# Performance work log

Measured on AMD Instinct MI355X. Metric: run time of the kernel, lower is better.

Reference implementation:

```python
import jax, jax.numpy as jnp
import numpy as np

N, E, G = 50000, 800000, 64
IN, EDGE = 128, 16
HID, H = 32, 4
FHID, HF = 64, 4
OUT = 16
NEG_SLOPE = 0.2


def _segment_softmax(logits, seg, num):
    m = jax.ops.segment_max(logits, seg, num_segments=num)
    m = jnp.where(jnp.isfinite(m), m, 0.0)
    p = jnp.exp(logits - m[seg])
    s = jax.ops.segment_sum(p, seg, num_segments=num)
    return p / (s[seg] + 1e-16)


def gatv2(x, src, dst, eattr, Wl, bl, Wr, br, We, att, bias, concat):
    # PyG GATv2Conv with add_self_loops=True (edge_attr fill_value='mean')
    n = x.shape[0]
    heads, ch = att.shape
    ones = jnp.ones((src.shape[0],), x.dtype)
    cnt = jax.ops.segment_sum(ones, dst, num_segments=n)
    mean_attr = jax.ops.segment_sum(eattr, dst, num_segments=n) / jnp.maximum(cnt, 1.0)[:, None]
    loop = jnp.arange(n)
    s = jnp.concatenate([src, loop])
    d = jnp.concatenate([dst, loop])
    ea = jnp.concatenate([eattr, mean_attr], axis=0)
    xl = (x @ Wl + bl).reshape(n, heads, ch)   # lin_l (source)
    xr = (x @ Wr + br).reshape(n, heads, ch)   # lin_r (target)
    ee = (ea @ We).reshape(-1, heads, ch)      # lin_edge (no bias)
    z = jax.nn.leaky_relu(xl[s] + xr[d] + ee, NEG_SLOPE)  # [E+N, H, C]
    logits = jnp.einsum('ehc,hc->eh', z, att)
    alpha = _segment_softmax(logits, d, n)
    out = jax.ops.segment_sum(alpha[:, :, None] * xl[s], d, num_segments=n)  # [N, H, C]
    out = out.reshape(n, heads * ch) if concat else out.mean(axis=1)
    return out + bias


def _forward(x, edge_attr, src, dst, batch,
             Wl0, bl0, Wr0, br0, We0, att0, bo0,
             Wlh, blh, Wrh, brh, Weh, atth, boh,
             Wlf, blf, Wrf, brf, Wef, attf, bof,
             Wlin, blin):
    h1 = jax.nn.relu(gatv2(x, src, dst, edge_attr, Wl0, bl0, Wr0, br0, We0, att0, bo0, True))
    h2 = jax.nn.relu(gatv2(h1, src, dst, edge_attr, Wlh, blh, Wrh, brh, Weh, atth, boh, True))
    h3 = jax.nn.relu(gatv2(h2, src, dst, edge_attr, Wlf, blf, Wrf, brf, Wef, attf, bof, False))
    # global_mean_pool over graphs
    gsum = jax.ops.segment_sum(h3, batch, num_segments=G)
    gcnt = jax.ops.segment_sum(jnp.ones((h3.shape[0],), h3.dtype), batch, num_segments=G)
    g = gsum / jnp.maximum(gcnt, 1.0)[:, None]
    return g @ Wlin + blin  # final_dropout inactive in eval mode


def setup_inputs():
    key = jax.random.key(0)
    ks = jax.random.split(key, 20)
    def p(i, shape, fan_in):
        return jax.random.normal(ks[i], shape, jnp.float32) / np.sqrt(fan_in)
    z = lambda *s: jnp.zeros(s, jnp.float32)
    return {
        'x': jax.random.normal(ks[0], (N, IN), jnp.float32),
        'edge_index': jax.random.randint(ks[1], (2, E), 0, N),
        'batch': jnp.sort(jax.random.randint(ks[2], (N,), 0, G)),
        'edge_attr': jax.random.normal(ks[3], (E, EDGE), jnp.float32),
        'Wl0': p(4, (IN, H * HID), IN), 'bl0': z(H * HID),
        'Wr0': p(5, (IN, H * HID), IN), 'br0': z(H * HID),
        'We0': p(6, (EDGE, H * HID), EDGE), 'att0': p(7, (H, HID), HID), 'bo0': z(H * HID),
        'Wlh': p(8, (H * HID, H * HID), H * HID), 'blh': z(H * HID),
        'Wrh': p(9, (H * HID, H * HID), H * HID), 'brh': z(H * HID),
        'Weh': p(10, (EDGE, H * HID), EDGE), 'atth': p(11, (H, HID), HID), 'boh': z(H * HID),
        'Wlf': p(12, (H * HID, HF * FHID), H * HID), 'blf': z(HF * FHID),
        'Wrf': p(13, (H * HID, HF * FHID), H * HID), 'brf': z(HF * FHID),
        'Wef': p(14, (EDGE, HF * FHID), EDGE), 'attf': p(15, (HF, FHID), FHID), 'bof': z(FHID),
        'Wlin': p(16, (FHID, OUT), FHID), 'blin': z(OUT),
    }


def reference(x, edge_index, batch, edge_attr, Wl0, bl0, Wr0, br0, We0, att0, bo0, Wlh, blh, Wrh, brh, Weh, atth, boh, Wlf, blf, Wrf, brf, Wef, attf, bof, Wlin, blin):
    return _forward(x, edge_attr, edge_index[0], edge_index[1], batch,
                    Wl0, bl0, Wr0, br0, We0, att0, bo0,
                    Wlh, blh, Wrh, brh, Weh, atth, boh,
                    Wlf, blf, Wrf, brf, Wef, attf, bof,
                    Wlin, blin)
```

## Files before the change

kernel.cpp:

```cpp
#include <hip/hip_runtime.h>
#include <cstddef>

#define NSLOPE 0.2f

constexpr int NN = 50000;
constexpr int EE = 800000;
constexpr int GG = 64;
constexpr int SCAN_B = 1024;

typedef unsigned short ushort_t;
typedef unsigned int uint_t;
typedef __bf16 bhalf;
typedef bhalf bhalf8 __attribute__((ext_vector_type(8)));
typedef float floatx4 __attribute__((ext_vector_type(4)));
typedef _Float16 half_t;
typedef half_t half2_t __attribute__((ext_vector_type(2)));

__device__ __forceinline__ ushort_t f2b(float f) {
  unsigned int u = __float_as_uint(f);
  unsigned int r = (u + 0x7fffu + ((u >> 16) & 1u)) >> 16;
  return (ushort_t)r;
}
__device__ __forceinline__ float b2f(ushort_t b) {
  return __uint_as_float(((unsigned int)b) << 16);
}
__device__ __forceinline__ uint_t packh2(float a, float b) {
  half2_t h = {(half_t)a, (half_t)b};
  return __builtin_bit_cast(uint_t, h);
}
__device__ __forceinline__ float dot2acc(uint_t ea, half2_t w, float c) {
  half2_t a = __builtin_bit_cast(half2_t, ea);
#if __has_builtin(__builtin_amdgcn_fdot2)
  return __builtin_amdgcn_fdot2(a, w, c, false);
#else
  return c + (float)a.x * (float)w.x + (float)a.y * (float)w.y;
#endif
}

__global__ void hist_kernel(const int* __restrict__ dst, int* __restrict__ hist, int E) {
  int e = blockIdx.x * blockDim.x + threadIdx.x;
  if (e < E) atomicAdd(&hist[dst[e]], 1);
}

__global__ void scan_block_kernel(const int* __restrict__ in, int* __restrict__ out,
                                  int* __restrict__ bsum, int n) {
  __shared__ int tmp[SCAN_B];
  int gid = blockIdx.x * SCAN_B + threadIdx.x;
  int v = (gid < n) ? in[gid] : 0;
  tmp[threadIdx.x] = v;
  __syncthreads();
  for (int off = 1; off < SCAN_B; off <<= 1) {
    int t = (threadIdx.x >= off) ? tmp[threadIdx.x - off] : 0;
    __syncthreads();
    tmp[threadIdx.x] += t;
    __syncthreads();
  }
  if (gid < n) out[gid] = tmp[threadIdx.x];
  if (threadIdx.x == SCAN_B - 1) bsum[blockIdx.x] = tmp[threadIdx.x];
}

__global__ void scan_totals_kernel(const int* __restrict__ bsum, int* __restrict__ boff, int nb) {
  if (blockIdx.x == 0 && threadIdx.x == 0) {
    int run = 0;
    for (int i = 0; i < nb; ++i) { boff[i] = run; run += bsum[i]; }
  }
}

__global__ void add_offsets_kernel(int* __restrict__ rowptr, const int* __restrict__ boff,
                                   int* __restrict__ cursor, int n) {
  int gid = blockIdx.x * SCAN_B + threadIdx.x;
  if (gid == 0) { rowptr[0] = 0; cursor[0] = 0; }
  if (gid < n) {
    int v = rowptr[1 + gid] + boff[blockIdx.x];
    rowptr[1 + gid] = v;
    if (1 + gid < n) cursor[1 + gid] = v;
  }
}

__global__ void scatter_fused_kernel(const int* __restrict__ dst, const int* __restrict__ src,
                                     const float* __restrict__ eattr, int* __restrict__ cursor,
                                     int* __restrict__ srcp, uint_t* __restrict__ eah, int E) {
  int e = blockIdx.x * blockDim.x + threadIdx.x;
  if (e >= E) return;
  const float4* a = reinterpret_cast<const float4*>(eattr + (size_t)e * 16);
  float4 f0 = a[0], f1 = a[1], f2 = a[2], f3 = a[3];
  int pos = atomicAdd(&cursor[dst[e]], 1);
  srcp[pos] = src[e];
  uint4 o0 = make_uint4(packh2(f0.x, f0.y), packh2(f0.z, f0.w),
                        packh2(f1.x, f1.y), packh2(f1.z, f1.w));
  uint4 o1 = make_uint4(packh2(f2.x, f2.y), packh2(f2.z, f2.w),
                        packh2(f3.x, f3.y), packh2(f3.z, f3.w));
  uint4* b = reinterpret_cast<uint4*>(eah + (size_t)pos * 8);
  b[0] = o0; b[1] = o1;
}

__global__ __launch_bounds__(256) void mean_attr_kernel(
    const int* __restrict__ rowptr, const uint_t* __restrict__ eah,
    uint_t* __restrict__ meanattr_h, int N) {
  const int lane = threadIdx.x & 63;
  int d = blockIdx.x * (blockDim.x >> 6) + (threadIdx.x >> 6);
  if (d >= N) return;
  int beg = rowptr[d], end = rowptr[d + 1];
  int k2 = lane & 7;
  int sub = lane >> 3;
  float ax = 0.f, ay = 0.f;
  for (int j = beg + sub; j < end; j += 8) {
    half2_t h = __builtin_bit_cast(half2_t, eah[(size_t)j * 8 + k2]);
    ax += (float)h.x; ay += (float)h.y;
  }
  ax += __shfl_xor(ax, 8);  ay += __shfl_xor(ay, 8);
  ax += __shfl_xor(ax, 16); ay += __shfl_xor(ay, 16);
  ax += __shfl_xor(ax, 32); ay += __shfl_xor(ay, 32);
  if (sub == 0) {
    int c = end - beg; if (c < 1) c = 1;
    float inv = 1.f / (float)c;
    meanattr_h[(size_t)d * 8 + k2] = packh2(ax * inv, ay * inv);
  }
}

__global__ void f2b_kernel(const float* __restrict__ in, ushort_t* __restrict__ out, int n4) {
  int i = blockIdx.x * blockDim.x + threadIdx.x;
  if (i >= n4) return;
  float4 v = reinterpret_cast<const float4*>(in)[i];
  ushort4 o = make_ushort4(f2b(v.x), f2b(v.y), f2b(v.z), f2b(v.w));
  reinterpret_cast<ushort4*>(out)[i] = o;
}

__global__ void prep_w_kernel(const float* W0, ushort_t* T0, int n0,
                              const float* W1, ushort_t* T1, int n1,
                              const float* W2, ushort_t* T2, int n2,
                              const float* W3, ushort_t* T3, int n3,
                              const float* W4, ushort_t* T4, int n4,
                              const float* W5, ushort_t* T5, int n5) {
  const float* W; ushort_t* T; int Nc;
  switch (blockIdx.y) {
    case 0: W = W0; T = T0; Nc = n0; break;
    case 1: W = W1; T = T1; Nc = n1; break;
    case 2: W = W2; T = T2; Nc = n2; break;
    case 3: W = W3; T = T3; Nc = n3; break;
    case 4: W = W4; T = T4; Nc = n4; break;
    default: W = W5; T = T5; Nc = n5; break;
  }
  int idx = blockIdx.x * blockDim.x + threadIdx.x;
  if (idx >= Nc * 128) return;
  int n = idx >> 7, k = idx & 127;
  T[idx] = f2b(W[(size_t)k * Nc + n]);
}

__global__ void prep_we_kernel(const float* We0, const float* att0, uint_t* w0, float* a0,
                               const float* We1, const float* att1, uint_t* w1, float* a1,
                               const float* We2, const float* att2, uint_t* w2, float* a2) {
  const float* We; const float* att; uint_t* wp; float* ap; int C;
  switch (blockIdx.y) {
    case 0: We = We0; att = att0; wp = w0; ap = a0; C = 128; break;
    case 1: We = We1; att = att1; wp = w1; ap = a1; C = 128; break;
    default: We = We2; att = att2; wp = w2; ap = a2; C = 256; break;
  }
  int idx = blockIdx.x * blockDim.x + threadIdx.x;
  if (idx >= 9 * C) return;
  if (idx < 8 * C) {
    int sh = (C == 256) ? 8 : 7;
    int k2 = idx >> sh, ch = idx & (C - 1);
    wp[idx] = packh2(We[(size_t)(2 * k2) * C + ch], We[(size_t)(2 * k2 + 1) * C + ch]);
  } else {
    int ch = idx - 8 * C;
    ap[ch] = att[ch] * 1.44269504f;
  }
}

__global__ __launch_bounds__(256) void gemm_bt_dual_bf16(
    const ushort_t* __restrict__ Xb,
    const ushort_t* __restrict__ Wt0, const float* __restrict__ b0, ushort_t* __restrict__ Y0,
    const ushort_t* __restrict__ Wt1, const float* __restrict__ b1, ushort_t* __restrict__ Y1,
    int M, int Nc) {
  constexpr int K = 128, BM = 128, LDT = 136;
  __shared__ ushort_t Als[BM * LDT];
  __shared__ ushort_t Bls[BM * LDT];
  int nb = Nc >> 7;
  int half = blockIdx.y / nb;
  int cb = blockIdx.y % nb;
  const ushort_t* Wt = half ? Wt1 : Wt0;
  const float* bias = half ? b1 : b0;
  ushort_t* Y = half ? Y1 : Y0;
  int r0 = blockIdx.x * BM;
  int col0 = cb * 128;
  int tid = threadIdx.x;
  {
    int rl = tid >> 5;
    int kq = (tid & 31) * 4;
#pragma unroll
    for (int s = 0; s < 16; ++s) {
      int row = rl + s * 8;
      int grow = r0 + row;
      ushort4 v = make_ushort4(0, 0, 0, 0);
      if (grow < M) v = *reinterpret_cast<const ushort4*>(Xb + (size_t)grow * K + kq);
      *reinterpret_cast<ushort4*>(&Als[row * LDT + kq]) = v;
      ushort4 wv = *reinterpret_cast<const ushort4*>(Wt + (size_t)(col0 + row) * K + kq);
      *reinterpret_cast<ushort4*>(&Bls[row * LDT + kq]) = wv;
    }
  }
  __syncthreads();
  int lane = tid & 63;
  int w = tid >> 6;
  int m0 = (w >> 1) * 64;
  int n0 = (w & 1) * 64;
  int rin = lane & 15, quad = lane >> 4;
  floatx4 acc[4][4];
#pragma unroll
  for (int i = 0; i < 4; ++i)
#pragma unroll
    for (int j = 0; j < 4; ++j) acc[i][j] = (floatx4){0.f, 0.f, 0.f, 0.f};
#pragma unroll
  for (int kt = 0; kt < 4; ++kt) {
    int ko = kt * 32 + quad * 8;
    bhalf8 af[4], bf[4];
#pragma unroll
    for (int i = 0; i < 4; ++i)
      af[i] = *reinterpret_cast<const bhalf8*>(&Als[(m0 + i * 16 + rin) * LDT + ko]);
#pragma unroll
    for (int i = 0; i < 4; ++i)
      bf[i] = *reinterpret_cast<const bhalf8*>(&Bls[(n0 + i * 16 + rin) * LDT + ko]);
#pragma unroll
    for (int mi = 0; mi < 4; ++mi)
#pragma unroll
      for (int ni = 0; ni < 4; ++ni)
        acc[mi][ni] = __builtin_amdgcn_mfma_f32_16x16x32_bf16(af[mi], bf[ni], acc[mi][ni], 0, 0, 0);
  }
#pragma unroll
  for (int ni = 0; ni < 4; ++ni) {
    int gcol = col0 + n0 + ni * 16 + rin;
    float bb = bias[gcol];
#pragma unroll
    for (int mi = 0; mi < 4; ++mi) {
      int growb = r0 + m0 + mi * 16 + quad * 4;
#pragma unroll
      for (int r = 0; r < 4; ++r) {
        int grow = growb + r;
        if (grow < M) Y[(size_t)grow * Nc + gcol] = f2b(acc[mi][ni][r] + bb);
      }
    }
  }
}

template <int VPL>
__device__ __forceinline__ void loadb(const ushort_t* p, float* v) {
  if constexpr (VPL == 2) {
    ushort2 t = *reinterpret_cast<const ushort2*>(p);
    v[0] = b2f(t.x); v[1] = b2f(t.y);
  } else {
    ushort4 t = *reinterpret_cast<const ushort4*>(p);
    v[0] = b2f(t.x); v[1] = b2f(t.y); v[2] = b2f(t.z); v[3] = b2f(t.w);
  }
}
template <int VPL>
__device__ __forceinline__ void storeb(ushort_t* p, const float* v) {
  if constexpr (VPL == 2) {
    *reinterpret_cast<ushort2*>(p) = make_ushort2(f2b(v[0]), f2b(v[1]));
  } else {
    *reinterpret_cast<ushort4*>(p) = make_ushort4(f2b(v[0]), f2b(v[1]), f2b(v[2]), f2b(v[3]));
  }
}

template <int VPL>
__device__ __forceinline__ void unpack_raw(const uint_t* raw, float* xv) {
#pragma unroll
  for (int r = 0; r < VPL / 2; ++r) {
    xv[2 * r]     = __uint_as_float(raw[r] << 16);
    xv[2 * r + 1] = __uint_as_float(raw[r] & 0xffff0000u);
  }
}

template <int VPL>
__device__ __forceinline__ float lrelu_dot(const float* xv, const float* rv,
                                           const half2_t (*wepk)[VPL], const float* areg,
                                           const uint_t* ea) {
  float part = 0.f;
#pragma unroll
  for (int j = 0; j < VPL; ++j) {
    float z = xv[j] + rv[j];
#pragma unroll
    for (int k2 = 0; k2 < 8; ++k2) z = dot2acc(ea[k2], wepk[k2][j], z);
    float zl = fmaxf(z, NSLOPE * z);
    part = fmaf(zl, areg[j], part);
  }
  part += __shfl_xor(part, 1);
  part += __shfl_xor(part, 2);
  part += __shfl_xor(part, 4);
  part += __shfl_xor(part, 8);
  return part;
}

template <int EB, int VPL>
__device__ __forceinline__ void load_grp(const int* __restrict__ srcp,
                                         const ushort_t* __restrict__ xl, int lane, int j,
                                         uint_t (*xraw)[VPL / 2]) {
  constexpr int RW = VPL / 2;
  int sn[EB];
#pragma unroll
  for (int u = 0; u < EB; ++u) sn[u] = srcp[j + u];
#pragma unroll
  for (int u = 0; u < EB; ++u) {
    const uint_t* p = reinterpret_cast<const uint_t*>(xl + (size_t)sn[u] * (VPL * 64)) + lane * RW;
#pragma unroll
    for (int r = 0; r < RW; ++r) xraw[u][r] = p[r];
  }
}

template <int EB, int VPL>
__device__ __forceinline__ void compute_grp(const uint_t* __restrict__ eah, int j,
                                            const uint_t (*xraw)[VPL / 2], int lane,
                                            const float* rv, const half2_t (*wepk)[VPL],
                                            const float* areg, float& s, float* acc) {
  float xv[EB][VPL];
#pragma unroll
  for (int u = 0; u < EB; ++u) unpack_raw<VPL>(xraw[u], xv[u]);
  float lg[EB];
#pragma unroll
  for (int u = 0; u < EB; ++u) {
    const uint_t* ap = eah + (size_t)(j + u) * 8;
    uint_t ea[8];
#pragma unroll
    for (int k2 = 0; k2 < 8; ++k2) ea[k2] = ap[k2];
    lg[u] = lrelu_dot<VPL>(xv[u], rv, wepk, areg, ea);
  }
  float p[EB], ps = 0.f;
#pragma unroll
  for (int u = 0; u < EB; ++u) { p[u] = exp2f(lg[u]); ps += p[u]; }
  s += ps;
#pragma unroll
  for (int jj = 0; jj < VPL; ++jj) {
    float t = p[0] * xv[0][jj];
#pragma unroll
    for (int u = 1; u < EB; ++u) t = fmaf(p[u], xv[u][jj], t);
    acc[jj] += t;
  }
}

template <int EB, int VPL, int C>
__device__ __forceinline__ void process_group(
    const int* __restrict__ srcp, const uint_t* __restrict__ eah, int j,
    const ushort_t* __restrict__ xl, int lane, const float* rv,
    const half2_t (*wepk)[VPL], const float* areg,
    float& s, float* acc) {
  uint_t xraw[EB][VPL / 2];
  load_grp<EB, VPL>(srcp, xl, lane, j, xraw);
  compute_grp<EB, VPL>(eah, j, xraw, lane, rv, wepk, areg, s, acc);
}

template <int VPL, int C>
__device__ __forceinline__ void process_edge(
    int sn, const uint_t* ea,
    const ushort_t* __restrict__ xl, int lane, const float* rv,
    const half2_t (*wepk)[VPL], const float* areg,
    float& s, float* acc) {
  float xv[VPL];
  loadb<VPL>(xl + (size_t)sn * C + lane * VPL, xv);
  float lg = lrelu_dot<VPL>(xv, rv, wepk, areg, ea);
  float p = exp2f(lg);
  s += p;
#pragma unroll
  for (int jj = 0; jj < VPL; ++jj) acc[jj] = fmaf(p, xv[jj], acc[jj]);
}

template <int C, bool FINAL>
__global__ __launch_bounds__(256) void gat_fused_kernel(
    const int* __restrict__ rowptr,
    const int* __restrict__ srcp, const uint_t* __restrict__ eah,
    const uint_t* __restrict__ meanattr_h,
    const ushort_t* __restrict__ xl, const ushort_t* __restrict__ xr,
    const uint_t* __restrict__ wep,
    const float* __restrict__ atts,
    const float* __restrict__ bias, ushort_t* __restrict__ hout, int N) {
  constexpr int VPL = C / 64;
  constexpr int RW = VPL / 2;
  constexpr int GEB = (C == 128) ? 8 : 4;
  const int lane = threadIdx.x & 63;
  int d = __builtin_amdgcn_readfirstlane(blockIdx.x * (blockDim.x >> 6) + (threadIdx.x >> 6));
  if (d >= N) return;

  half2_t wepk[8][VPL];
  float areg[VPL];
#pragma unroll
  for (int k2 = 0; k2 < 8; ++k2)
#pragma unroll
    for (int jj = 0; jj < VPL; ++jj)
      wepk[k2][jj] = __builtin_bit_cast(half2_t, wep[k2 * C + lane * VPL + jj]);
#pragma unroll
  for (int jj = 0; jj < VPL; ++jj) areg[jj] = atts[lane * VPL + jj];

  int beg = rowptr[d], end = rowptr[d + 1];
  float rv[VPL];
  loadb<VPL>(xr + (size_t)d * C + lane * VPL, rv);

  float s = 0.f;
  float acc[VPL];
#pragma unroll
  for (int jj = 0; jj < VPL; ++jj) acc[jj] = 0.f;

  int j = beg;
  for (; j + 2 * GEB <= end; j += 2 * GEB) {
    uint_t xa[GEB][RW], xb[GEB][RW];
    load_grp<GEB, VPL>(srcp, xl, lane, j, xa);
    load_grp<GEB, VPL>(srcp, xl, lane, j + GEB, xb);
    compute_grp<GEB, VPL>(eah, j, xa, lane, rv, wepk, areg, s, acc);
    compute_grp<GEB, VPL>(eah, j + GEB, xb, lane, rv, wepk, areg, s, acc);
  }
  for (; j + GEB <= end; j += GEB) {
    uint_t xa[GEB][RW];
    load_grp<GEB, VPL>(srcp, xl, lane, j, xa);
    compute_grp<GEB, VPL>(eah, j, xa, lane, rv, wepk, areg, s, acc);
  }
  if constexpr (C == 128) {
    for (; j + 4 <= end; j += 4)
      process_group<4, VPL, C>(srcp, eah, j, xl, lane, rv, wepk, areg, s, acc);
  }
  for (; j + 2 <= end; j += 2)
    process_group<2, VPL, C>(srcp, eah, j, xl, lane, rv, wepk, areg, s, acc);
  for (; j < end; ++j)
    process_group<1, VPL, C>(srcp, eah, j, xl, lane, rv, wepk, areg, s, acc);

  {
    const uint_t* mp = meanattr_h + (size_t)d * 8;
    uint_t ea[8];
#pragma unroll
    for (int k2 = 0; k2 < 8; ++k2) ea[k2] = mp[k2];
    process_edge<VPL, C>(d, ea, xl, lane, rv, wepk, areg, s, acc);
  }

  float inv = 1.f / (s + 1e-16f);
  if constexpr (!FINAL) {
    float res[VPL];
#pragma unroll
    for (int jj = 0; jj < VPL; ++jj) {
      float v = acc[jj] * inv + bias[lane * VPL + jj];
      res[jj] = v > 0.f ? v : 0.f;
    }
    storeb<VPL>(hout + (size_t)d * C + lane * VPL, res);
  } else {
    float v[VPL];
#pragma unroll
    for (int jj = 0; jj < VPL; ++jj) v[jj] = acc[jj] * inv;
#pragma unroll
    for (int jj = 0; jj < VPL; ++jj) {
      v[jj] += __shfl_xor(v[jj], 16);
      v[jj] += __shfl_xor(v[jj], 32);
    }
    if (lane < 16) {
      float res[VPL];
#pragma unroll
      for (int jj = 0; jj < VPL; ++jj) {
        float val = 0.25f * v[jj] + bias[lane * VPL + jj];
        res[jj] = val > 0.f ? val : 0.f;
      }
      storeb<VPL>(hout + (size_t)d * 64 + lane * VPL, res);
    }
  }
}

__global__ __launch_bounds__(256) void pool_kernel(
    const ushort_t* __restrict__ h3, const int* __restrict__ batch,
    float* __restrict__ gsum, float* __restrict__ gcnt, int N) {
  const int lane = threadIdx.x & 63;
  const int w = blockIdx.x * (blockDim.x >> 6) + (threadIdx.x >> 6);
  const int nw = gridDim.x * (blockDim.x >> 6);
  const int chunk = (N + nw - 1) / nw;
  int i0 = w * chunk;
  int i1 = i0 + chunk; if (i1 > N) i1 = N;
  if (i0 >= i1) return;
  int cur = batch[i0];
  float acc = 0.f;
  int cnt = 0;
  for (int i = i0; i < i1; ++i) {
    int g = batch[i];
    if (g != cur) {
      atomicAdd(&gsum[(size_t)cur * 64 + lane], acc);
      if (lane == 0) atomicAdd(&gcnt[cur], (float)cnt);
      acc = 0.f; cnt = 0; cur = g;
    }
    acc += b2f(h3[(size_t)i * 64 + lane]);
    ++cnt;
  }
  atomicAdd(&gsum[(size_t)cur * 64 + lane], acc);
  if (lane == 0) atomicAdd(&gcnt[cur], (float)cnt);
}

__global__ void final_kernel(const float* __restrict__ gsum, const float* __restrict__ gcnt,
                             const float* __restrict__ Wlin, const float* __restrict__ blin,
                             float* __restrict__ out) {
  int idx = blockIdx.x * blockDim.x + threadIdx.x;
  if (idx >= GG * 16) return;
  int g = idx >> 4, o = idx & 15;
  float c = gcnt[g];
  c = c > 1.f ? c : 1.f;
  float inv = 1.f / c;
  float acc = blin[o];
  for (int f = 0; f < 64; ++f) acc = fmaf(gsum[(size_t)g * 64 + f] * inv, Wlin[f * 16 + o], acc);
  out[idx] = acc;
}

extern "C" void kernel_launch(void* const* d_in, const int* in_sizes, int n_in,
                              void* d_out, int out_size, void* d_ws, size_t ws_size,
                              hipStream_t stream) {
  (void)in_sizes; (void)n_in; (void)out_size; (void)ws_size;
  const float* x     = (const float*)d_in[0];
  const int*   eidx  = (const int*)d_in[1];
  const int*   batch = (const int*)d_in[2];
  const float* eattr = (const float*)d_in[3];
  const float* Wl0 = (const float*)d_in[4];  const float* bl0 = (const float*)d_in[5];
  const float* Wr0 = (const float*)d_in[6];  const float* br0 = (const float*)d_in[7];
  const float* We0 = (const float*)d_in[8];  const float* att0 = (const float*)d_in[9];
  const float* bo0 = (const float*)d_in[10];
  const float* Wlh = (const float*)d_in[11]; const float* blh = (const float*)d_in[12];
  const float* Wrh = (const float*)d_in[13]; const float* brh = (const float*)d_in[14];
  const float* Weh = (const float*)d_in[15]; const float* atth = (const float*)d_in[16];
  const float* boh = (const float*)d_in[17];
  const float* Wlf = (const float*)d_in[18]; const float* blf = (const float*)d_in[19];
  const float* Wrf = (const float*)d_in[20]; const float* brf = (const float*)d_in[21];
  const float* Wef = (const float*)d_in[22]; const float* attf = (const float*)d_in[23];
  const float* bof = (const float*)d_in[24];
  const float* Wlin = (const float*)d_in[25]; const float* blin = (const float*)d_in[26];

  const int* src = eidx;
  const int* dst = eidx + EE;

  char* ws = (char*)d_ws;
  size_t off = 0;
  auto take = [&](size_t bytes) -> void* {
    void* p = ws + off;
    off += (bytes + 1023) & ~(size_t)1023;
    return p;
  };
  ushort_t* xl     = (ushort_t*)take((size_t)NN * 256 * 2);
  ushort_t* xr     = (ushort_t*)take((size_t)NN * 256 * 2);
  ushort_t* hb     = (ushort_t*)take((size_t)NN * 128 * 2);
  ushort_t* xb     = (ushort_t*)take((size_t)NN * 128 * 2);
  uint_t* meanattr_h = (uint_t*)take((size_t)NN * 8 * 4);
  int* hist        = (int*)take((size_t)NN * 4);
  int* rowptr      = (int*)take((size_t)(NN + 1) * 4);
  int* cursor      = (int*)take((size_t)NN * 4);
  int* bsum        = (int*)take(256);
  int* boff        = (int*)take(256);
  float* gsum      = (float*)take((size_t)GG * 64 * 4);
  float* gcnt      = (float*)take((size_t)GG * 4);
  ushort_t* wtl0   = (ushort_t*)take((size_t)128 * 128 * 2);
  ushort_t* wtr0   = (ushort_t*)take((size_t)128 * 128 * 2);
  ushort_t* wtlh   = (ushort_t*)take((size_t)128 * 128 * 2);
  ushort_t* wtrh   = (ushort_t*)take((size_t)128 * 128 * 2);
  ushort_t* wtlf   = (ushort_t*)take((size_t)256 * 128 * 2);
  ushort_t* wtrf   = (ushort_t*)take((size_t)256 * 128 * 2);
  int* srcp        = (int*)take((size_t)EE * 4);
  uint_t* eah      = (uint_t*)take((size_t)EE * 8 * 4);
  uint_t* we0p     = (uint_t*)take((size_t)8 * 128 * 4);
  uint_t* wehp     = (uint_t*)take((size_t)8 * 128 * 4);
  uint_t* wefp     = (uint_t*)take((size_t)8 * 256 * 4);
  float* att0s     = (float*)take((size_t)128 * 4);
  float* atths     = (float*)take((size_t)128 * 4);
  float* attfs     = (float*)take((size_t)256 * 4);

  hipMemsetAsync(hist, 0, (size_t)NN * 4, stream);
  hipMemsetAsync(gsum, 0, (size_t)GG * 64 * 4, stream);
  hipMemsetAsync(gcnt, 0, (size_t)GG * 4, stream);
  hist_kernel<<<(EE + 255) / 256, 256, 0, stream>>>(dst, hist, EE);
  int nsb = (NN + SCAN_B - 1) / SCAN_B;
  scan_block_kernel<<<nsb, SCAN_B, 0, stream>>>(hist, rowptr + 1, bsum, NN);
  scan_totals_kernel<<<1, 64, 0, stream>>>(bsum, boff, nsb);
  add_offsets_kernel<<<nsb, SCAN_B, 0, stream>>>(rowptr, boff, cursor, NN);
  scatter_fused_kernel<<<(EE + 255) / 256, 256, 0, stream>>>(dst, src, eattr, cursor, srcp, eah, EE);
  mean_attr_kernel<<<(NN + 3) / 4, 256, 0, stream>>>(rowptr, eah, meanattr_h, NN);
  prep_w_kernel<<<dim3(128, 6), 256, 0, stream>>>(Wl0, wtl0, 128, Wr0, wtr0, 128,
                                                  Wlh, wtlh, 128, Wrh, wtrh, 128,
                                                  Wlf, wtlf, 256, Wrf, wtrf, 256);
  prep_we_kernel<<<dim3(9, 3), 256, 0, stream>>>(We0, att0, we0p, att0s,
                                                 Weh, atth, wehp, atths,
                                                 Wef, attf, wefp, attfs);
  f2b_kernel<<<(NN * 128 / 4 + 255) / 256, 256, 0, stream>>>(x, xb, NN * 128 / 4);

  const int AGG_BLOCKS = (NN + 3) / 4;
  const int GEMM_MB = (NN + 127) / 128;

  gemm_bt_dual_bf16<<<dim3(GEMM_MB, 2), 256, 0, stream>>>(xb, wtl0, bl0, xl, wtr0, br0, xr, NN, 128);
  gat_fused_kernel<128, false><<<AGG_BLOCKS, 256, 0, stream>>>(
      rowptr, srcp, eah, meanattr_h, xl, xr, we0p, att0s, bo0, hb, NN);
  gemm_bt_dual_bf16<<<dim3(GEMM_MB, 2), 256, 0, stream>>>(hb, wtlh, blh, xl, wtrh, brh, xr, NN, 128);
  gat_fused_kernel<128, false><<<AGG_BLOCKS, 256, 0, stream>>>(
      rowptr, srcp, eah, meanattr_h, xl, xr, wehp, atths, boh, hb, NN);
  gemm_bt_dual_bf16<<<dim3(GEMM_MB, 4), 256, 0, stream>>>(hb, wtlf, blf, xl, wtrf, brf, xr, NN, 256);
  gat_fused_kernel<256, true><<<AGG_BLOCKS, 256, 0, stream>>>(
      rowptr, srcp, eah, meanattr_h, xl, xr, wefp, attfs, bof, hb, NN);
  pool_kernel<<<128, 256, 0, stream>>>(hb, batch, gsum, gcnt, NN);
  final_kernel<<<4, 256, 0, stream>>>(gsum, gcnt, Wlin, blin, (float*)d_out);
}
```

Measured before the change: 733.5 us.

## Replace shuffle reductions with DPP, vectorize edge-attr loads, simplify edge batching

New measurement: 694.1 us. 1.06x faster.

```diff
diff --git a/kernel.cpp b/kernel.cpp
--- a/kernel.cpp
+++ b/kernel.cpp
@@ -35,6 +35,18 @@
 #else
   return c + (float)a.x * (float)w.x + (float)a.y * (float)w.y;
 #endif
+}
+
+__device__ __forceinline__ float red16(float x) {
+  int v = __builtin_bit_cast(int, x);
+  x += __builtin_bit_cast(float, __builtin_amdgcn_update_dpp(0, v, 0xB1, 0xF, 0xF, true));
+  v = __builtin_bit_cast(int, x);
+  x += __builtin_bit_cast(float, __builtin_amdgcn_update_dpp(0, v, 0x4E, 0xF, 0xF, true));
+  v = __builtin_bit_cast(int, x);
+  x += __builtin_bit_cast(float, __builtin_amdgcn_update_dpp(0, v, 0x124, 0xF, 0xF, true));
+  v = __builtin_bit_cast(int, x);
+  x += __builtin_bit_cast(float, __builtin_amdgcn_update_dpp(0, v, 0x128, 0xF, 0xF, true));
+  return x;
 }
 
 __global__ void hist_kernel(const int* __restrict__ dst, int* __restrict__ hist, int E) {
@@ -262,15 +274,6 @@
 }
 
 template <int VPL>
-__device__ __forceinline__ void unpack_raw(const uint_t* raw, float* xv) {
-#pragma unroll
-  for (int r = 0; r < VPL / 2; ++r) {
-    xv[2 * r]     = __uint_as_float(raw[r] << 16);
-    xv[2 * r + 1] = __uint_as_float(raw[r] & 0xffff0000u);
-  }
-}
-
-template <int VPL>
 __device__ __forceinline__ float lrelu_dot(const float* xv, const float* rv,
                                            const half2_t (*wepk)[VPL], const float* areg,
                                            const uint_t* ea) {
@@ -283,57 +286,7 @@
     float zl = fmaxf(z, NSLOPE * z);
     part = fmaf(zl, areg[j], part);
   }
-  part += __shfl_xor(part, 1);
-  part += __shfl_xor(part, 2);
-  part += __shfl_xor(part, 4);
-  part += __shfl_xor(part, 8);
-  return part;
-}
-
-template <int EB, int VPL>
-__device__ __forceinline__ void load_grp(const int* __restrict__ srcp,
-                                         const ushort_t* __restrict__ xl, int lane, int j,
-                                         uint_t (*xraw)[VPL / 2]) {
-  constexpr int RW = VPL / 2;
-  int sn[EB];
-#pragma unroll
-  for (int u = 0; u < EB; ++u) sn[u] = srcp[j + u];
-#pragma unroll
-  for (int u = 0; u < EB; ++u) {
-    const uint_t* p = reinterpret_cast<const uint_t*>(xl + (size_t)sn[u] * (VPL * 64)) + lane * RW;
-#pragma unroll
-    for (int r = 0; r < RW; ++r) xraw[u][r] = p[r];
-  }
-}
-
-template <int EB, int VPL>
-__device__ __forceinline__ void compute_grp(const uint_t* __restrict__ eah, int j,
-                                            const uint_t (*xraw)[VPL / 2], int lane,
-                                            const float* rv, const half2_t (*wepk)[VPL],
-                                            const float* areg, float& s, float* acc) {
-  float xv[EB][VPL];
-#pragma unroll
-  for (int u = 0; u < EB; ++u) unpack_raw<VPL>(xraw[u], xv[u]);
-  float lg[EB];
-#pragma unroll
-  for (int u = 0; u < EB; ++u) {
-    const uint_t* ap = eah + (size_t)(j + u) * 8;
-    uint_t ea[8];
-#pragma unroll
-    for (int k2 = 0; k2 < 8; ++k2) ea[k2] = ap[k2];
-    lg[u] = lrelu_dot<VPL>(xv[u], rv, wepk, areg, ea);
-  }
-  float p[EB], ps = 0.f;
-#pragma unroll
-  for (int u = 0; u < EB; ++u) { p[u] = exp2f(lg[u]); ps += p[u]; }
-  s += ps;
-#pragma unroll
-  for (int jj = 0; jj < VPL; ++jj) {
-    float t = p[0] * xv[0][jj];
-#pragma unroll
-    for (int u = 1; u < EB; ++u) t = fmaf(p[u], xv[u][jj], t);
-    acc[jj] += t;
-  }
+  return red16(part);
 }
 
 template <int EB, int VPL, int C>
@@ -342,9 +295,31 @@
     const ushort_t* __restrict__ xl, int lane, const float* rv,
     const half2_t (*wepk)[VPL], const float* areg,
     float& s, float* acc) {
-  uint_t xraw[EB][VPL / 2];
-  load_grp<EB, VPL>(srcp, xl, lane, j, xraw);
-  compute_grp<EB, VPL>(eah, j, xraw, lane, rv, wepk, areg, s, acc);
+  int sn[EB];
+#pragma unroll
+  for (int u = 0; u < EB; ++u) sn[u] = srcp[j + u];
+  float xv[EB][VPL];
+#pragma unroll
+  for (int u = 0; u < EB; ++u) loadb<VPL>(xl + (size_t)sn[u] * C + lane * VPL, xv[u]);
+  float lg[EB];
+#pragma unroll
+  for (int u = 0; u < EB; ++u) {
+    const uint4* ap4 = reinterpret_cast<const uint4*>(eah + (size_t)(j + u) * 8);
+    uint4 e0 = ap4[0], e1 = ap4[1];
+    uint_t ea[8] = {e0.x, e0.y, e0.z, e0.w, e1.x, e1.y, e1.z, e1.w};
+    lg[u] = lrelu_dot<VPL>(xv[u], rv, wepk, areg, ea);
+  }
+  float p[EB], ps = 0.f;
+#pragma unroll
+  for (int u = 0; u < EB; ++u) { p[u] = exp2f(lg[u]); ps += p[u]; }
+  s += ps;
+#pragma unroll
+  for (int jj = 0; jj < VPL; ++jj) {
+    float t = p[0] * xv[0][jj];
+#pragma unroll
+    for (int u = 1; u < EB; ++u) t = fmaf(p[u], xv[u][jj], t);
+    acc[jj] += t;
+  }
 }
 
 template <int VPL, int C>
@@ -372,8 +347,6 @@
     const float* __restrict__ atts,
     const float* __restrict__ bias, ushort_t* __restrict__ hout, int N) {
   constexpr int VPL = C / 64;
-  constexpr int RW = VPL / 2;
-  constexpr int GEB = (C == 128) ? 8 : 4;
   const int lane = threadIdx.x & 63;
   int d = __builtin_amdgcn_readfirstlane(blockIdx.x * (blockDim.x >> 6) + (threadIdx.x >> 6));
   if (d >= N) return;
@@ -398,32 +371,21 @@
   for (int jj = 0; jj < VPL; ++jj) acc[jj] = 0.f;
 
   int j = beg;
-  for (; j + 2 * GEB <= end; j += 2 * GEB) {
-    uint_t xa[GEB][RW], xb[GEB][RW];
-    load_grp<GEB, VPL>(srcp, xl, lane, j, xa);
-    load_grp<GEB, VPL>(srcp, xl, lane, j + GEB, xb);
-    compute_grp<GEB, VPL>(eah, j, xa, lane, rv, wepk, areg, s, acc);
-    compute_grp<GEB, VPL>(eah, j + GEB, xb, lane, rv, wepk, areg, s, acc);
-  }
-  for (; j + GEB <= end; j += GEB) {
-    uint_t xa[GEB][RW];
-    load_grp<GEB, VPL>(srcp, xl, lane, j, xa);
-    compute_grp<GEB, VPL>(eah, j, xa, lane, rv, wepk, areg, s, acc);
-  }
   if constexpr (C == 128) {
-    for (; j + 4 <= end; j += 4)
-      process_group<4, VPL, C>(srcp, eah, j, xl, lane, rv, wepk, areg, s, acc);
-  }
+    for (; j + 8 <= end; j += 8)
+      process_group<8, VPL, C>(srcp, eah, j, xl, lane, rv, wepk, areg, s, acc);
+  }
+  for (; j + 4 <= end; j += 4)
+    process_group<4, VPL, C>(srcp, eah, j, xl, lane, rv, wepk, areg, s, acc);
   for (; j + 2 <= end; j += 2)
     process_group<2, VPL, C>(srcp, eah, j, xl, lane, rv, wepk, areg, s, acc);
   for (; j < end; ++j)
     process_group<1, VPL, C>(srcp, eah, j, xl, lane, rv, wepk, areg, s, acc);
 
   {
-    const uint_t* mp = meanattr_h + (size_t)d * 8;
-    uint_t ea[8];
-#pragma unroll
-    for (int k2 = 0; k2 < 8; ++k2) ea[k2] = mp[k2];
+    const uint4* mp4 = reinterpret_cast<const uint4*>(meanattr_h + (size_t)d * 8);
+    uint4 e0 = mp4[0], e1 = mp4[1];
+    uint_t ea[8] = {e0.x, e0.y, e0.z, e0.w, e1.x, e1.y, e1.z, e1.w};
     process_edge<VPL, C>(d, ea, xl, lane, rv, wepk, areg, s, acc);
   }
 
```
